# Optimization experiments

Measured on AMD Instinct MI355X. Metric: run time of the kernel, lower is better.

Reference implementation:

```python
import jax, jax.numpy as jnp
import numpy as np

N, C, H, W = 8, 256, 128, 128
HD = 256          # hidden_depth
FC, FS, CS = 8, 2, 8  # heads_count, fold_size, center_size
EPS_GN = 1e-5


def setup_inputs() -> dict:
    key = jax.random.key(0)
    ks = jax.random.split(key, 8)
    d = {
        'x': jax.random.normal(ks[0], (N, C, H, W), jnp.float32),
        'proj_w': jax.random.normal(ks[1], (2 * HD, C), jnp.float32) * 0.02,
        'proj_b': jnp.zeros((2 * HD,), jnp.float32),
        'merge_w': jax.random.normal(ks[2], (C, HD), jnp.float32) * 0.02,
        'merge_b': jnp.zeros((C,), jnp.float32),
        'alpha': jnp.ones((1,), jnp.float32),
        'beta': jnp.zeros((1,), jnp.float32),
        'g0_w': jnp.ones((C,), jnp.float32),
        'g0_b': jnp.zeros((C,), jnp.float32),
        'mlp_w0': jax.random.normal(ks[3], (2 * C, 2 * C), jnp.float32) * 0.02,
        'mlp_b0': jnp.zeros((2 * C,), jnp.float32),
        'mlp_w1': jax.random.normal(ks[4], (2 * C, C), jnp.float32) * 0.02,
        'mlp_b1': jnp.zeros((C,), jnp.float32),
        'g1_w': jnp.ones((C,), jnp.float32),
        'g1_b': jnp.zeros((C,), jnp.float32),
        'layer_scale': jnp.full((C,), 1e-5, jnp.float32),
    }
    return d


def _group_norm1(x, w, b):
    # GroupNorm(1, C): normalize over (C,H,W) per sample, per-channel affine
    mu = x.mean(axis=(1, 2, 3), keepdims=True)
    var = ((x - mu) ** 2).mean(axis=(1, 2, 3), keepdims=True)
    xn = (x - mu) * jax.lax.rsqrt(var + EPS_GN)
    return xn * w[None, :, None, None] + b[None, :, None, None]


def _l2norm(v):
    return v / jnp.maximum(jnp.linalg.norm(v, axis=-1, keepdims=True), 1e-12)


def _local_cluster(x, proj_w, proj_b, merge_w, merge_b, alpha, beta):
    n = x.shape[0]
    # 1x1 conv proj: C -> 2*HD
    y = jnp.einsum('nchw,oc->nohw', x, proj_w) + proj_b[None, :, None, None]
    c = y.shape[1] // FC              # per-head channels (2*HD/FC)
    h, w = H // FS, W // FS
    # 'n (fc c) (fh h) (fw w) -> (n fc fh fw) c h w'
    y = y.reshape(n, FC, c, FS, h, FS, w).transpose(0, 1, 3, 5, 2, 4, 6)
    y = y.reshape(n * FC * FS * FS, c, h, w)
    m = y.shape[0]
    # adaptive avg pool to CSxCS (h,w divisible by CS -> uniform pooling)
    center = y.reshape(m, c, CS, h // CS, CS, w // CS).mean(axis=(3, 5))
    L, s = h * w, CS * CS
    yf = y.reshape(m, c, L).transpose(0, 2, 1)       # [m, L, c]
    cf = center.reshape(m, c, s).transpose(0, 2, 1)  # [m, s, c]
    cv = c // 2
    x_point, x_value = yf[..., :cv], yf[..., cv:]
    c_point, c_value = cf[..., :cv], cf[..., cv:]
    sim = jnp.einsum('mlc,msc->mls', _l2norm(x_point), _l2norm(c_point))
    sim = jax.nn.sigmoid(alpha * sim + beta)         # [m, L, s]
    vals = sim.max(axis=2)                           # [m, L]
    idx = sim.argmax(axis=2) + s * jnp.arange(m)[:, None]
    vals = vals.reshape(-1)
    idx = idx.reshape(-1)
    xv = x_value.reshape(-1, cv)
    cvv = c_value.reshape(-1, cv)
    xv_aug = jnp.concatenate([xv, jnp.ones((xv.shape[0], 1), xv.dtype)], axis=1)
    cv_aug = jnp.concatenate([cvv, jnp.ones((cvv.shape[0], 1), cvv.dtype)], axis=1)
    # scatter-add weighted points into centers
    nc = cv_aug.at[idx].add(vals[:, None] * xv_aug)
    nc = nc[:, :-1] / nc[:, -1:]
    # gather back
    nx = vals[:, None] * nc[idx]                     # [m*L, cv]
    # '(n fc fh fw h w) c -> n (fc c) (fh h) (fw w)'
    nx = nx.reshape(n, FC, FS, FS, h, w, cv).transpose(0, 1, 6, 2, 4, 3, 5)
    nx = nx.reshape(n, FC * cv, H, W)                # [n, HD, H, W]
    return jnp.einsum('nchw,oc->nohw', nx, merge_w) + merge_b[None, :, None, None]


def reference(x, proj_w, proj_b, merge_w, merge_b, alpha, beta, g0_w, g0_b,
              mlp_w0, mlp_b0, mlp_w1, mlp_b1, g1_w, g1_b, layer_scale):
    new_x = _local_cluster(x, proj_w, proj_b, merge_w, merge_b, alpha, beta)
    new_x = _group_norm1(new_x, g0_w, g0_b)
    t = jnp.concatenate([x, new_x], axis=1)          # [n, 2C, H, W]
    t = t.transpose(0, 2, 3, 1)                      # NHWC
    t = jax.nn.gelu(t @ mlp_w0 + mlp_b0, approximate=False)
    t = t @ mlp_w1 + mlp_b1
    t = t.transpose(0, 3, 1, 2)                      # NCHW
    t = _group_norm1(t, g1_w, g1_b)
    t = t * layer_scale[None, :, None, None]
    return t + x
```

## Files before the change

### kernel.cpp

```cpp
#include <hip/hip_runtime.h>
#include <math.h>

#define PIX   16384
#define NB    8
#define CIN   256

typedef __attribute__((ext_vector_type(8))) short    short8;
typedef __attribute__((ext_vector_type(4))) float    f32x4;
typedef __attribute__((ext_vector_type(4))) unsigned short us4;
typedef __attribute__((ext_vector_type(8))) unsigned short us8;
typedef __attribute__((ext_vector_type(4))) unsigned char uc4;

__device__ __forceinline__ float bf2f(unsigned short h) {
  return __uint_as_float(((unsigned int)h) << 16);
}
__device__ __forceinline__ unsigned short f2bf(float f) {
  unsigned int u = __float_as_uint(f);
  return (unsigned short)((u + 0x7FFFu + ((u >> 16) & 1u)) >> 16);
}
__device__ __forceinline__ float gelu_f(float v) {
  return 0.5f * v * (1.f + erff(v * 0.70710678118654752f));
}

__device__ __forceinline__ unsigned fmono(float f) {
  const unsigned u = __float_as_uint(f);
  return (u & 0x80000000u) ? ~u : (u | 0x80000000u);
}

__device__ __forceinline__ unsigned umax16(unsigned v) {
  unsigned t;
  t = (unsigned)__builtin_amdgcn_update_dpp((int)v, (int)v, 0x121, 0xF, 0xF, false); v = v > t ? v : t;
  t = (unsigned)__builtin_amdgcn_update_dpp((int)v, (int)v, 0x122, 0xF, 0xF, false); v = v > t ? v : t;
  t = (unsigned)__builtin_amdgcn_update_dpp((int)v, (int)v, 0x124, 0xF, 0xF, false); v = v > t ? v : t;
  t = (unsigned)__builtin_amdgcn_update_dpp((int)v, (int)v, 0x128, 0xF, 0xF, false); v = v > t ? v : t;
  return v;
}
__device__ __forceinline__ int imin16(int v) {
  int t;
  t = __builtin_amdgcn_update_dpp(v, v, 0x121, 0xF, 0xF, false); v = v < t ? v : t;
  t = __builtin_amdgcn_update_dpp(v, v, 0x122, 0xF, 0xF, false); v = v < t ? v : t;
  t = __builtin_amdgcn_update_dpp(v, v, 0x124, 0xF, 0xF, false); v = v < t ? v : t;
  t = __builtin_amdgcn_update_dpp(v, v, 0x128, 0xF, 0xF, false); v = v < t ? v : t;
  return v;
}

__global__ void zero_kernel(float* p, int n) {
  int i = blockIdx.x * blockDim.x + threadIdx.x;
  if (i < n) p[i] = 0.f;
}

__global__ void prep_weights(const float* __restrict__ pw_f, const float* __restrict__ mw_f,
                             const float* __restrict__ w0, const float* __restrict__ w1,
                             unsigned short* __restrict__ pw, unsigned short* __restrict__ mw,
                             unsigned short* __restrict__ w0t, unsigned short* __restrict__ w1t) {
  const int S1 = 512 * 256, S2 = 256 * 256, S3 = 512 * 512, S4 = 256 * 512;
  int i = blockIdx.x * 256 + threadIdx.x;
  if (i < S1) { pw[i] = f2bf(pw_f[i]); return; }
  i -= S1;
  if (i < S2) { mw[i] = f2bf(mw_f[i]); return; }
  i -= S2;
  if (i < S3) { int o = i >> 9, k = i & 511; w0t[i] = f2bf(w0[k * 512 + o]); return; }
  i -= S3;
  if (i < S4) { int o = i >> 9, k = i & 511; w1t[i] = f2bf(w1[k * 256 + o]); }
}

__global__ __launch_bounds__(256) void x_to_nhwc(const float* __restrict__ x,
                                                 unsigned short* __restrict__ xT) {
  __shared__ float tile[64][65];
  const int t = threadIdx.x;
  const int p0 = blockIdx.x * 64, c0 = blockIdx.y * 64, n = blockIdx.z;
#pragma unroll
  for (int i = 0; i < 4; i++) {
    const int c = i * 16 + (t >> 4);
    const float4 v = *(const float4*)(x + ((size_t)(n * 256 + c0 + c) << 14) + p0 + (t & 15) * 4);
    tile[c][(t & 15) * 4]     = v.x;
    tile[c][(t & 15) * 4 + 1] = v.y;
    tile[c][(t & 15) * 4 + 2] = v.z;
    tile[c][(t & 15) * 4 + 3] = v.w;
  }
  __syncthreads();
#pragma unroll
  for (int i = 0; i < 4; i++) {
    const int pp = i * 16 + (t >> 4);
    const int cl = (t & 15) * 4;
    us4 o;
    o.x = f2bf(tile[cl][pp]); o.y = f2bf(tile[cl + 1][pp]);
    o.z = f2bf(tile[cl + 2][pp]); o.w = f2bf(tile[cl + 3][pp]);
    *(us4*)&xT[(((size_t)n << 14) + p0 + pp) * 256 + c0 + cl] = o;
  }
}

template<bool CONCAT, bool GELU, bool STATS>
__global__ __launch_bounds__(256, 4) void mfma_gemm(
    const unsigned short* __restrict__ A, const float* __restrict__ bias,
    const unsigned short* __restrict__ B1, const unsigned short* __restrict__ B2,
    unsigned short* __restrict__ Y, int M, int K, int K1,
    int astride, int bstride, float* __restrict__ sums) {
  __shared__ unsigned short As[8192];
  __shared__ unsigned short Bs[8192];
  __shared__ float r1[4], r2[4];
  const int t = threadIdx.x;
  const int lane = t & 63, w = t >> 6;
  const int quad = lane >> 4, l16 = lane & 15;
  const int p0 = blockIdx.x * 128, m0 = blockIdx.y * 128;
  const int n = blockIdx.z;
  const int wm = w & 1, wn = w >> 1;
  const int K2 = K - K1;

  A += (size_t)n * astride;

  f32x4 acc[4][4];
#pragma unroll
  for (int im = 0; im < 4; im++)
#pragma unroll
    for (int in = 0; in < 4; in++) acc[im][in] = (f32x4)0.f;

  for (int k0 = 0; k0 < K; k0 += 64) {
    __syncthreads();
#pragma unroll
    for (int i = 0; i < 4; i++) {
      const int c = (w << 2) | i;
      const int tm = c >> 1, kk = c & 1;
      const int krow = k0 + kk * 32 + quad * 8;
      const unsigned short* ga = A + (size_t)(m0 + tm * 16 + l16) * K + krow;
      __builtin_amdgcn_global_load_lds((const __attribute__((address_space(1))) void*)ga,
          (__attribute__((address_space(3))) void*)&As[c * 512], 16, 0, 0);
      const int prow = p0 + tm * 16 + l16;
      const unsigned short* gb;
      if (!CONCAT || krow < K1)
        gb = B1 + ((((size_t)n << 14) + prow) * (size_t)K1) + krow;
      else
        gb = B2 + ((((size_t)n << 14) + prow) * (size_t)K2) + (krow - K1);
      __builtin_amdgcn_global_load_lds((const __attribute__((address_space(1))) void*)gb,
          (__attribute__((address_space(3))) void*)&Bs[c * 512], 16, 0, 0);
    }
    __syncthreads();
#pragma unroll
    for (int kk = 0; kk < 2; kk++) {
      short8 af[4], bfr[4];
#pragma unroll
      for (int im = 0; im < 4; im++)
        af[im] = *(const short8*)&As[(((wm * 4 + im) * 2 + kk) * 64 + lane) * 8];
#pragma unroll
      for (int in = 0; in < 4; in++)
        bfr[in] = *(const short8*)&Bs[(((wn * 4 + in) * 2 + kk) * 64 + lane) * 8];
#pragma unroll
      for (int im = 0; im < 4; im++)
#pragma unroll
        for (int in = 0; in < 4; in++)
          acc[im][in] = __builtin_amdgcn_mfma_f32_16x16x32_bf16(af[im], bfr[in], acc[im][in], 0, 0, 0);
    }
  }

  const size_t nb = ((size_t)n << 14);
  float s = 0.f, s2 = 0.f;
#pragma unroll
  for (int im = 0; im < 4; im++) {
    const int om = m0 + (wm * 4 + im) * 16 + quad * 4;
    const f32x4 bv = *(const f32x4*)(bias + (size_t)n * bstride + om);
#pragma unroll
    for (int in = 0; in < 4; in++) {
      const int p = p0 + (wn * 4 + in) * 16 + l16;
      float v0 = acc[im][in].x + bv.x;
      float v1 = acc[im][in].y + bv.y;
      float v2 = acc[im][in].z + bv.z;
      float v3 = acc[im][in].w + bv.w;
      if (GELU) { v0 = gelu_f(v0); v1 = gelu_f(v1); v2 = gelu_f(v2); v3 = gelu_f(v3); }
      if (STATS) {
        s += (v0 + v1) + (v2 + v3);
        s2 = fmaf(v0, v0, s2); s2 = fmaf(v1, v1, s2);
        s2 = fmaf(v2, v2, s2); s2 = fmaf(v3, v3, s2);
      }
      us4 o4;
      o4.x = f2bf(v0); o4.y = f2bf(v1); o4.z = f2bf(v2); o4.w = f2bf(v3);
      *(us4*)&Y[(nb + p) * M + om] = o4;
    }
  }
  if (STATS) {
#pragma unroll
    for (int off = 32; off > 0; off >>= 1) {
      s += __shfl_down(s, off);
      s2 += __shfl_down(s2, off);
    }
    if (lane == 0) { r1[w] = s; r2[w] = s2; }
    __syncthreads();
    if (t == 0) {
      atomicAdd(&sums[2 * n],     (r1[0] + r1[1]) + (r1[2] + r1[3]));
      atomicAdd(&sums[2 * n + 1], (r2[0] + r2[1]) + (r2[2] + r2[3]));
    }
  }
}


__global__ __launch_bounds__(256) void centers_kernel(
    const unsigned short* __restrict__ y, unsigned short* __restrict__ cpnh_g,
    float* __restrict__ cval_g) {
  const int m = blockIdx.y, slice = blockIdx.x;
  const int n = m >> 5, f = (m >> 2) & 7, s1 = (m >> 1) & 1, s2 = m & 1;
  const int t = threadIdx.x;
  __shared__ float cs[16][68];

  const size_t nbase = ((size_t)n << 14);
  const int prow0 = s1 * 64, pcol0 = s2 * 64, ch0 = f * 64;

  {
    const int bl = t >> 4;
    const int b = slice * 16 + bl;
    const int tid = t & 15, cg = tid & 7, ph = tid >> 3;
    const int pr0 = prow0 + (b >> 3) * 8 + ph * 4;
    const int pc0 = pcol0 + (b & 7) * 8;
    const unsigned short* yb = y + (nbase + (size_t)pr0 * 128 + pc0) * 512 + ch0 + cg * 8;
    float a8[8] = {0.f, 0.f, 0.f, 0.f, 0.f, 0.f, 0.f, 0.f};
#pragma unroll
    for (int r = 0; r < 4; r++) {
      us8 buf[8];
#pragma unroll
      for (int cc = 0; cc < 8; cc++)
        buf[cc] = *(const us8*)(yb + ((size_t)r * 128 + cc) * 512);
#pragma unroll
      for (int cc = 0; cc < 8; cc++)
#pragma unroll
        for (int j = 0; j < 8; j++) a8[j] += bf2f(buf[cc][j]);
    }
#pragma unroll
    for (int j = 0; j < 8; j++) a8[j] += __shfl_xor(a8[j], 8);
    if (ph == 0) {
      f32x4 o0, o1;
      o0.x = a8[0] * (1.f / 64.f); o0.y = a8[1] * (1.f / 64.f);
      o0.z = a8[2] * (1.f / 64.f); o0.w = a8[3] * (1.f / 64.f);
      o1.x = a8[4] * (1.f / 64.f); o1.y = a8[5] * (1.f / 64.f);
      o1.z = a8[6] * (1.f / 64.f); o1.w = a8[7] * (1.f / 64.f);
      *(f32x4*)&cs[bl][cg * 8]     = o0;
      *(f32x4*)&cs[bl][cg * 8 + 4] = o1;
    }
  }
  __syncthreads();

  if (t < 128) {
    const int bl = t >> 3, jg = t & 7;
    const int bg = slice * 16 + bl;
    if (jg < 8) {
      f32x4 ov;
      ov.x = cs[bl][32 + jg * 4]; ov.y = cs[bl][32 + jg * 4 + 1];
      ov.z = cs[bl][32 + jg * 4 + 2]; ov.w = cs[bl][32 + jg * 4 + 3];
      *(f32x4*)&cval_g[((size_t)(m * 64 + bg) << 5) + jg * 4] = ov;
    }
    float s = 0.f;
#pragma unroll
    for (int cc = 0; cc < 32; cc++) { const float v = cs[bl][cc]; s = fmaf(v, v, s); }
    const float inv = 1.f / fmaxf(sqrtf(s), 1e-12f);
    us4 o;
    o.x = f2bf(cs[bl][jg * 4] * inv);     o.y = f2bf(cs[bl][jg * 4 + 1] * inv);
    o.z = f2bf(cs[bl][jg * 4 + 2] * inv); o.w = f2bf(cs[bl][jg * 4 + 3] * inv);
    *(us4*)&cpnh_g[((size_t)(m * 64 + bg) << 5) + jg * 4] = o;
  }
}

__global__ __launch_bounds__(256, 4) void assign_kernel(
    const unsigned short* __restrict__ y, const unsigned short* __restrict__ cpnh_g,
    const float* __restrict__ alpha_p, const float* __restrict__ beta_p,
    float* __restrict__ svals_g, unsigned char* __restrict__ sbest_g,
    float* __restrict__ accp_v, float* __restrict__ accp_c) {
  const int m = blockIdx.y, slice = blockIdx.x;
  const int n = m >> 5, f = (m >> 2) & 7, s1 = (m >> 1) & 1, s2 = m & 1;
  const int t = threadIdx.x;
  const int wave = t >> 6, lane = t & 63;
  const int quad = lane >> 4, l16 = lane & 15;
  const float alpha = alpha_p[0], beta = beta_p[0];

  __shared__ unsigned short yvs[512][34];
  __shared__ float svalss[512];
  __shared__ unsigned char sidxs[512];

  const size_t nbase = ((size_t)n << 14);
  const int prow0 = s1 * 64, pcol0 = s2 * 64, ch0 = f * 64;

  const short8 cb0 = *(const short8*)&cpnh_g[((size_t)(m * 64 +  0 + l16) << 5) + quad * 8];
  const short8 cb1 = *(const short8*)&cpnh_g[((size_t)(m * 64 + 16 + l16) << 5) + quad * 8];
  const short8 cb2 = *(const short8*)&cpnh_g[((size_t)(m * 64 + 32 + l16) << 5) + quad * 8];
  const short8 cb3 = *(const short8*)&cpnh_g[((size_t)(m * 64 + 48 + l16) << 5) + quad * 8];
  const int sl4 = (((l16 >> 2) << 4) | (l16 & 3)) << 2;

  auto loadpt = [&](int tile, short8& a, short8& v) {
    const int pidx = slice * 512 + wave * 128 + tile * 16;
    const int pix = (prow0 + (pidx >> 6)) * 128 + pcol0 + (pidx & 63) + l16;
    const unsigned short* yp = y + (nbase + pix) * 512 + ch0 + quad * 8;
    a = *(const short8*)yp;
    v = *(const short8*)(yp + 32);
  };

  auto compute_tile = [&](int tile, short8 apt, short8 avl) {
    const int pl = wave * 128 + tile * 16 + l16;
    const int pidx = slice * 512 + pl;

    float nrm = 0.f;
#pragma unroll
    for (int j = 0; j < 8; j++) {
      const float fv = bf2f((unsigned short)apt[j]);
      nrm = fmaf(fv, fv, nrm);
    }
    nrm += __shfl_xor(nrm, 16);
    nrm += __shfl_xor(nrm, 32);
    const float inva = 1.f / fmaxf(sqrtf(nrm), 1e-12f);

    const f32x4 d0 = __builtin_amdgcn_mfma_f32_16x16x32_bf16(apt, cb0, (f32x4)0.f, 0, 0, 0);
    const f32x4 d1 = __builtin_amdgcn_mfma_f32_16x16x32_bf16(apt, cb1, (f32x4)0.f, 0, 0, 0);
    const f32x4 d2 = __builtin_amdgcn_mfma_f32_16x16x32_bf16(apt, cb2, (f32x4)0.f, 0, 0, 0);
    const f32x4 d3 = __builtin_amdgcn_mfma_f32_16x16x32_bf16(apt, cb3, (f32x4)0.f, 0, 0, 0);

    float bv[4]; int bi[4];
#pragma unroll
    for (int r = 0; r < 4; r++) {
      const unsigned u0 = fmono(d0[r]);
      const unsigned u1 = fmono(d1[r]);
      const unsigned u2 = fmono(d2[r]);
      const unsigned u3 = fmono(d3[r]);
      unsigned mx = u0 > u1 ? u0 : u1;
      const unsigned mxb = u2 > u3 ? u2 : u3;
      mx = mx > mxb ? mx : mxb;
      mx = umax16(mx);
      int c0 = (u0 == mx) ? l16        : 64;
      int c1 = (u1 == mx) ? (16 + l16) : 64;
      int c2 = (u2 == mx) ? (32 + l16) : 64;
      int c3 = (u3 == mx) ? (48 + l16) : 64;
      int ci = c0 < c1 ? c0 : c1;
      const int cb = c2 < c3 ? c2 : c3;
      ci = ci < cb ? ci : cb;
      ci = imin16(ci);
      bi[r] = ci;
      bv[r] = __uint_as_float((mx & 0x80000000u) ? (mx ^ 0x80000000u) : ~mx);
    }

    const float rv01 = (l16 & 1) ? bv[1] : bv[0];
    const float rv23 = (l16 & 1) ? bv[3] : bv[2];
    const float rowv = (l16 & 2) ? rv23 : rv01;
    const int   ri01 = (l16 & 1) ? bi[1] : bi[0];
    const int   ri23 = (l16 & 1) ? bi[3] : bi[2];
    const int   rowi = (l16 & 2) ? ri23 : ri01;
    const unsigned pk = (__float_as_uint(rowv) & ~63u) | (unsigned)rowi;
    const unsigned got = (unsigned)__builtin_amdgcn_ds_bpermute(sl4, (int)pk);
    const int   idx = (int)(got & 63u);
    const float dot = __uint_as_float(got & ~63u);

    const float val = 1.f / (1.f + __expf(-fmaf(alpha, dot * inva, beta)));
    if (quad == 0) {
      svals_g[(size_t)m * 4096 + pidx + 0] = val;
      sbest_g[(size_t)m * 4096 + pidx + 0] = (unsigned char)idx;
      svalss[pl] = val;
      sidxs[pl] = (unsigned char)idx;
    }
    *(short8*)&yvs[pl][quad * 8] = avl;
  };

  {
    short8 a0, v0, a1, v1, a2, v2, a3, v3, a4, v4, a5, v5, a6, v6, a7, v7;
    loadpt(0, a0, v0); loadpt(1, a1, v1); loadpt(2, a2, v2); loadpt(3, a3, v3);
    loadpt(4, a4, v4); loadpt(5, a5, v5); loadpt(6, a6, v6); loadpt(7, a7, v7);
    compute_tile(0, a0, v0); compute_tile(1, a1, v1);
    compute_tile(2, a2, v2); compute_tile(3, a3, v3);
    compute_tile(4, a4, v4); compute_tile(5, a5, v5);
    compute_tile(6, a6, v6); compute_tile(7, a7, v7);
  }
  __syncthreads();

  {
    const int b = t >> 2, g = t & 3;
    float a8[8] = {0.f, 0.f, 0.f, 0.f, 0.f, 0.f, 0.f, 0.f};
    float ac = 0.f;
#pragma unroll 4
    for (int p4 = 0; p4 < 128; p4++) {
      const uc4 i4 = *(const uc4*)&sidxs[p4 * 4];
#pragma unroll
      for (int u = 0; u < 4; u++) {
        const int idx = (u == 0) ? i4.x : (u == 1) ? i4.y : (u == 2) ? i4.z : i4.w;
        if (idx == b) {
          const int p = p4 * 4 + u;
          const float val = svalss[p];
          const us8 yv = *(const us8*)&yvs[p][g * 8];
#pragma unroll
          for (int j = 0; j < 8; j++) a8[j] = fmaf(val, bf2f(yv[j]), a8[j]);
          ac += val;
        }
      }
    }
    const size_t pb = ((size_t)(m * 8 + slice)) * 64;
    f32x4 o0, o1;
    o0.x = a8[0]; o0.y = a8[1]; o0.z = a8[2]; o0.w = a8[3];
    o1.x = a8[4]; o1.y = a8[5]; o1.z = a8[6]; o1.w = a8[7];
    *(f32x4*)&accp_v[(pb + b) * 32 + g * 8]     = o0;
    *(f32x4*)&accp_v[(pb + b) * 32 + g * 8 + 4] = o1;
    if (g == 0) accp_c[pb + b] = ac;
  }
}

__global__ __launch_bounds__(256) void gather_kernel(
    const float* __restrict__ accp_v, const float* __restrict__ accp_c,
    const float* __restrict__ cval_g, const float* __restrict__ svals_g,
    const unsigned char* __restrict__ sbest_g, unsigned short* __restrict__ nx) {
  const int m = blockIdx.y, slice = blockIdx.x;
  const int n = m >> 5, f = (m >> 2) & 7, s1 = (m >> 1) & 1, s2 = m & 1;
  const int t = threadIdx.x;
  __shared__ float cm[64][34];

  const size_t nbase = ((size_t)n << 14);
  const int prow0 = s1 * 64, pcol0 = s2 * 64;

  for (int i = t; i < 2048; i += 256) {
    const int b = i >> 5, q = i & 31;
    float s = cval_g[((size_t)(m * 64 + b) << 5) + q];
    float c = 1.f;
#pragma unroll
    for (int s8 = 0; s8 < 8; s8++) {
      const size_t pb = ((size_t)(m * 8 + s8)) * 64 + b;
      s += accp_v[pb * 32 + q];
      c += accp_c[pb];
    }
    cm[b][q] = s / c;
  }
  __syncthreads();

#pragma unroll
  for (int pass = 0; pass < 2; pass++) {
    const int l = slice * 512 + pass * 256 + t;
    const int p = (prow0 + (l >> 6)) * 128 + pcol0 + (l & 63);
    const float v = svals_g[(size_t)m * 4096 + l];
    const int b = sbest_g[(size_t)m * 4096 + l];
    unsigned short* nr = nx + (nbase + p) * 256 + f * 32;
#pragma unroll
    for (int q8 = 0; q8 < 4; q8++) {
      const float2 a0 = *(const float2*)&cm[b][q8 * 8];
      const float2 a1 = *(const float2*)&cm[b][q8 * 8 + 2];
      const float2 a2 = *(const float2*)&cm[b][q8 * 8 + 4];
      const float2 a3 = *(const float2*)&cm[b][q8 * 8 + 6];
      us8 o;
      o[0] = f2bf(v * a0.x); o[1] = f2bf(v * a0.y);
      o[2] = f2bf(v * a1.x); o[3] = f2bf(v * a1.y);
      o[4] = f2bf(v * a2.x); o[5] = f2bf(v * a2.y);
      o[6] = f2bf(v * a3.x); o[7] = f2bf(v * a3.y);
      *(us8*)&nr[q8 * 8] = o;
    }
  }
}

__global__ void gn_finalize0(const float* __restrict__ sums, const float* __restrict__ g0w,
                             const float* __restrict__ g0b, float* __restrict__ scl,
                             float* __restrict__ bia) {
  const int n = blockIdx.x, c = threadIdx.x;
  const float cntinv = 1.f / (float)(CIN * PIX);
  const float mu = sums[2 * n] * cntinv;
  const float var = sums[2 * n + 1] * cntinv - mu * mu;
  const float rs = rsqrtf(var + 1e-5f);
  const float a = rs * g0w[c];
  scl[n * 256 + c] = a;
  bia[n * 256 + c] = g0b[c] - mu * a;
}

__global__ void w0_scale(const unsigned short* __restrict__ w0t,
                         const float* __restrict__ scl, unsigned short* __restrict__ w0s) {
  const int n = blockIdx.y;
  const int i = blockIdx.x * 256 + threadIdx.x;
  const int k = i & 511;
  unsigned short v = w0t[i];
  if (k >= 256) v = f2bf(bf2f(v) * scl[n * 256 + k - 256]);
  w0s[(size_t)n * 262144 + i] = v;
}

__global__ void b0_eff(const unsigned short* __restrict__ w0t, const float* __restrict__ b0,
                       const float* __restrict__ bia, float* __restrict__ b0e) {
  const int n = blockIdx.y;
  const int o = blockIdx.x * 256 + threadIdx.x;
  float s = b0[o];
  const unsigned short* wr = w0t + (size_t)o * 512 + 256;
  const float* br = bia + n * 256;
#pragma unroll 4
  for (int k = 0; k < 256; k++) s = fmaf(bf2f(wr[k]), br[k], s);
  b0e[n * 512 + o] = s;
}

__global__ __launch_bounds__(256) void final_transpose(
    const unsigned short* __restrict__ u, const float* __restrict__ x,
    const float* __restrict__ sums, const float* __restrict__ g1w,
    const float* __restrict__ g1b, const float* __restrict__ lsc,
    float* __restrict__ out) {
  __shared__ float tile[64][68];
  const int t = threadIdx.x;
  const int p0 = blockIdx.x * 64, c0 = blockIdx.y * 64, n = blockIdx.z;
  {
    const int pl = t >> 2, g = t & 3;
    const unsigned short* up = u + ((((size_t)n << 14) + p0 + pl) << 8) + c0 + g * 16;
    const us8 v0 = *(const us8*)up;
    const us8 v1 = *(const us8*)(up + 8);
#pragma unroll
    for (int j = 0; j < 8; j++) {
      tile[pl][g * 16 + j] = bf2f(v0[j]);
      tile[pl][g * 16 + 8 + j] = bf2f(v1[j]);
    }
  }
  __syncthreads();
  {
    const int cl = t >> 2, g = t & 3;
    const int c = c0 + cl;
    const float cntinv = 1.f / (float)(CIN * PIX);
    const float mu = sums[2 * n] * cntinv;
    const float var = sums[2 * n + 1] * cntinv - mu * mu;
    const float rs = rsqrtf(var + 1e-5f);
    const float gw = rs * g1w[c] * lsc[c];
    const float gb = (g1b[c] - mu * rs * g1w[c]) * lsc[c];
    const size_t rowb = ((size_t)(n * 256 + c) << 14) + p0 + g * 16;
#pragma unroll
    for (int q = 0; q < 4; q++) {
      const float4 xv = *(const float4*)(x + rowb + q * 4);
      float4 o;
      o.x = fmaf(tile[g * 16 + q * 4][cl], gw, gb) + xv.x;
      o.y = fmaf(tile[g * 16 + q * 4 + 1][cl], gw, gb) + xv.y;
      o.z = fmaf(tile[g * 16 + q * 4 + 2][cl], gw, gb) + xv.z;
      o.w = fmaf(tile[g * 16 + q * 4 + 3][cl], gw, gb) + xv.w;
      *(float4*)(out + rowb + q * 4) = o;
    }
  }
}

extern "C" void kernel_launch(void* const* d_in, const int* in_sizes, int n_in,
                              void* d_out, int out_size, void* d_ws, size_t ws_size,
                              hipStream_t stream) {
  const float* x       = (const float*)d_in[0];
  const float* proj_w  = (const float*)d_in[1];
  const float* proj_b  = (const float*)d_in[2];
  const float* merge_w = (const float*)d_in[3];
  const float* merge_b = (const float*)d_in[4];
  const float* alpha   = (const float*)d_in[5];
  const float* beta    = (const float*)d_in[6];
  const float* g0w     = (const float*)d_in[7];
  const float* g0b     = (const float*)d_in[8];
  const float* w0      = (const float*)d_in[9];
  const float* b0      = (const float*)d_in[10];
  const float* w1      = (const float*)d_in[11];
  const float* b1      = (const float*)d_in[12];
  const float* g1w     = (const float*)d_in[13];
  const float* g1b     = (const float*)d_in[14];
  const float* lsc     = (const float*)d_in[15];
  float* out = (float*)d_out;

  unsigned short* wsu = (unsigned short*)d_ws;
  unsigned short* xT  = wsu;
  unsigned short* y   = xT + (size_t)33554432;
  unsigned short* nx  = y + (size_t)67108864;
  unsigned short* pw  = nx + (size_t)33554432;
  unsigned short* mw  = pw + 131072;
  unsigned short* w0t = mw + 65536;
  unsigned short* w1t = w0t + 262144;
  unsigned short* w0s = w1t + 131072;
  float* sums = (float*)(w0s + (size_t)2097152);
  float* scl0 = sums + 32;
  float* bia0 = scl0 + 2048;
  float* b0e  = bia0 + 2048;
  unsigned short* newx = (unsigned short*)d_out;

  float* svals_g = (float*)((char*)d_out + 67108864);
  float* cval_g  = svals_g + 1048576;
  float* accp_v  = cval_g + 524288;
  float* accp_c  = accp_v + 4194304;
  unsigned short* cpnh_g = (unsigned short*)(accp_c + 131072);
  unsigned char*  sbest_g = (unsigned char*)(cpnh_g + 524288);

  zero_kernel<<<1, 64, 0, stream>>>(sums, 32);
  prep_weights<<<2304, 256, 0, stream>>>(proj_w, merge_w, w0, w1, pw, mw, w0t, w1t);
  x_to_nhwc<<<dim3(256, 4, NB), 256, 0, stream>>>(x, xT);

  mfma_gemm<false, false, false><<<dim3(128, 4, NB), 256, 0, stream>>>(
      pw, proj_b, xT, nullptr, y, 512, 256, 256, 0, 0, nullptr);

  centers_kernel<<<dim3(4, 256), 256, 0, stream>>>(y, cpnh_g, cval_g);
  assign_kernel<<<dim3(8, 256), 256, 0, stream>>>(
      y, cpnh_g, alpha, beta, svals_g, sbest_g, accp_v, accp_c);
  gather_kernel<<<dim3(8, 256), 256, 0, stream>>>(
      accp_v, accp_c, cval_g, svals_g, sbest_g, nx);

  mfma_gemm<false, false, true><<<dim3(128, 2, NB), 256, 0, stream>>>(
      mw, merge_b, nx, nullptr, newx, 256, 256, 256, 0, 0, sums);

  gn_finalize0<<<NB, 256, 0, stream>>>(sums, g0w, g0b, scl0, bia0);
  w0_scale<<<dim3(1024, NB), 256, 0, stream>>>(w0t, scl0, w0s);
  b0_eff<<<dim3(2, NB), 256, 0, stream>>>(w0t, b0, bia0, b0e);

  mfma_gemm<true, true, false><<<dim3(128, 4, NB), 256, 0, stream>>>(
      w0s, b0e, xT, newx, y, 512, 512, 256, 262144, 512, nullptr);

  mfma_gemm<false, false, true><<<dim3(128, 2, NB), 256, 0, stream>>>(
      w1t, b1, y, nullptr, nx, 256, 512, 512, 0, 0, sums + 16);

  final_transpose<<<dim3(256, 4, NB), 256, 0, stream>>>(
      nx, x, sums + 16, g1w, g1b, lsc, out);
}
```

Measured before the change: 915.4 us.

## Fuse projection GEMM into cluster assign kernel and compute centers from pooled input

```diff
diff --git a/kernel.cpp b/kernel.cpp
--- a/kernel.cpp
+++ b/kernel.cpp
@@ -52,8 +52,9 @@
 __global__ void prep_weights(const float* __restrict__ pw_f, const float* __restrict__ mw_f,
                              const float* __restrict__ w0, const float* __restrict__ w1,
                              unsigned short* __restrict__ pw, unsigned short* __restrict__ mw,
-                             unsigned short* __restrict__ w0t, unsigned short* __restrict__ w1t) {
-  const int S1 = 512 * 256, S2 = 256 * 256, S3 = 512 * 512, S4 = 256 * 512;
+                             unsigned short* __restrict__ w0t, unsigned short* __restrict__ w1t,
+                             unsigned short* __restrict__ pwF) {
+  const int S1 = 512 * 256, S2 = 256 * 256, S3 = 512 * 512, S4 = 256 * 512, S5 = 512 * 256;
   int i = blockIdx.x * 256 + threadIdx.x;
   if (i < S1) { pw[i] = f2bf(pw_f[i]); return; }
   i -= S1;
@@ -61,7 +62,14 @@
   i -= S2;
   if (i < S3) { int o = i >> 9, k = i & 511; w0t[i] = f2bf(w0[k * 512 + o]); return; }
   i -= S3;
-  if (i < S4) { int o = i >> 9, k = i & 511; w1t[i] = f2bf(w1[k * 256 + o]); }
+  if (i < S4) { int o = i >> 9, k = i & 511; w1t[i] = f2bf(w1[k * 256 + o]); return; }
+  i -= S4;
+  if (i < S5) {
+    const int j = i & 7, lane = (i >> 3) & 63, ks = (i >> 9) & 7, ct = (i >> 12) & 3, f = i >> 14;
+    const int ch = f * 64 + ct * 16 + (lane & 15);
+    const int k  = ks * 32 + (lane >> 4) * 8 + j;
+    pwF[i] = f2bf(pw_f[ch * 256 + k]);
+  }
 }
 
 __global__ __launch_bounds__(256) void x_to_nhwc(const float* __restrict__ x,
@@ -192,72 +200,94 @@
 }
 
 
+__global__ __launch_bounds__(256) void xmeans_kernel(
+    const unsigned short* __restrict__ xT, float* __restrict__ xmean) {
+  const int reg = blockIdx.y, ksl = blockIdx.x;
+  const int nn = reg >> 2, s1 = (reg >> 1) & 1, s2 = reg & 1;
+  const int t = threadIdx.x;
+  const int b = t >> 2, kq = t & 3;
+  const int k0 = ksl * 64 + kq * 16;
+  const size_t nbase = ((size_t)nn << 14);
+  const int pr0 = s1 * 64 + (b >> 3) * 8, pc0 = s2 * 64 + (b & 7) * 8;
+  float a16[16];
+#pragma unroll
+  for (int j = 0; j < 16; j++) a16[j] = 0.f;
+#pragma unroll 1
+  for (int r = 0; r < 8; r++) {
+#pragma unroll
+    for (int c = 0; c < 8; c++) {
+      const unsigned short* xp = xT + (nbase + (size_t)(pr0 + r) * 128 + pc0 + c) * 256 + k0;
+      const us8 v0 = *(const us8*)xp;
+      const us8 v1 = *(const us8*)(xp + 8);
+#pragma unroll
+      for (int j = 0; j < 8; j++) {
+        a16[j]     += bf2f(v0[j]);
+        a16[8 + j] += bf2f(v1[j]);
+      }
+    }
+  }
+  float* o = xmean + (((size_t)(reg * 64 + b)) << 8) + k0;
+#pragma unroll
+  for (int j = 0; j < 16; j++) o[j] = a16[j] * (1.f / 64.f);
+}
+
 __global__ __launch_bounds__(256) void centers_kernel(
-    const unsigned short* __restrict__ y, unsigned short* __restrict__ cpnh_g,
+    const float* __restrict__ xmean, const unsigned short* __restrict__ pw,
+    const float* __restrict__ proj_bp, unsigned short* __restrict__ cpnh_g,
     float* __restrict__ cval_g) {
-  const int m = blockIdx.y, slice = blockIdx.x;
-  const int n = m >> 5, f = (m >> 2) & 7, s1 = (m >> 1) & 1, s2 = m & 1;
+  const int m = blockIdx.x;
+  const int nn = m >> 5, f = (m >> 2) & 7, s1 = (m >> 1) & 1, s2 = m & 1;
+  const int reg = (nn << 2) | (s1 << 1) | s2;
   const int t = threadIdx.x;
-  __shared__ float cs[16][68];
-
-  const size_t nbase = ((size_t)n << 14);
-  const int prow0 = s1 * 64, pcol0 = s2 * 64, ch0 = f * 64;
+  const int b = t >> 2, cg = t & 3;
+  __shared__ float cs[64][68];
 
   {
-    const int bl = t >> 4;
-    const int b = slice * 16 + bl;
-    const int tid = t & 15, cg = tid & 7, ph = tid >> 3;
-    const int pr0 = prow0 + (b >> 3) * 8 + ph * 4;
-    const int pc0 = pcol0 + (b & 7) * 8;
-    const unsigned short* yb = y + (nbase + (size_t)pr0 * 128 + pc0) * 512 + ch0 + cg * 8;
-    float a8[8] = {0.f, 0.f, 0.f, 0.f, 0.f, 0.f, 0.f, 0.f};
-#pragma unroll
-    for (int r = 0; r < 4; r++) {
-      us8 buf[8];
-#pragma unroll
-      for (int cc = 0; cc < 8; cc++)
-        buf[cc] = *(const us8*)(yb + ((size_t)r * 128 + cc) * 512);
-#pragma unroll
-      for (int cc = 0; cc < 8; cc++)
-#pragma unroll
-        for (int j = 0; j < 8; j++) a8[j] += bf2f(buf[cc][j]);
-    }
-#pragma unroll
-    for (int j = 0; j < 8; j++) a8[j] += __shfl_xor(a8[j], 8);
-    if (ph == 0) {
-      f32x4 o0, o1;
-      o0.x = a8[0] * (1.f / 64.f); o0.y = a8[1] * (1.f / 64.f);
-      o0.z = a8[2] * (1.f / 64.f); o0.w = a8[3] * (1.f / 64.f);
-      o1.x = a8[4] * (1.f / 64.f); o1.y = a8[5] * (1.f / 64.f);
-      o1.z = a8[6] * (1.f / 64.f); o1.w = a8[7] * (1.f / 64.f);
-      *(f32x4*)&cs[bl][cg * 8]     = o0;
-      *(f32x4*)&cs[bl][cg * 8 + 4] = o1;
-    }
+    const float* xm = xmean + (((size_t)(reg * 64 + b)) << 8);
+    float acc16[16];
+#pragma unroll
+    for (int c = 0; c < 16; c++) acc16[c] = 0.f;
+#pragma unroll 1
+    for (int k = 0; k < 256; k += 8) {
+      float xv[8];
+#pragma unroll
+      for (int j = 0; j < 8; j++) xv[j] = xm[k + j];
+#pragma unroll
+      for (int c = 0; c < 16; c++) {
+        const us8 wv = *(const us8*)(pw + (size_t)(f * 64 + cg * 16 + c) * 256 + k);
+#pragma unroll
+        for (int j = 0; j < 8; j++) acc16[c] = fmaf(bf2f(wv[j]), xv[j], acc16[c]);
+      }
+    }
+#pragma unroll
+    for (int c = 0; c < 16; c++)
+      cs[b][cg * 16 + c] = acc16[c] + proj_bp[f * 64 + cg * 16 + c];
   }
   __syncthreads();
 
-  if (t < 128) {
-    const int bl = t >> 3, jg = t & 7;
-    const int bg = slice * 16 + bl;
-    if (jg < 8) {
-      f32x4 ov;
-      ov.x = cs[bl][32 + jg * 4]; ov.y = cs[bl][32 + jg * 4 + 1];
-      ov.z = cs[bl][32 + jg * 4 + 2]; ov.w = cs[bl][32 + jg * 4 + 3];
-      *(f32x4*)&cval_g[((size_t)(m * 64 + bg) << 5) + jg * 4] = ov;
-    }
+  {
+    const int b2 = t >> 2, jg = t & 3;
+    const f32x4 ov0 = *(const f32x4*)&cs[b2][32 + jg * 8];
+    const f32x4 ov1 = *(const f32x4*)&cs[b2][32 + jg * 8 + 4];
+    *(f32x4*)&cval_g[(((size_t)(m * 64 + b2)) << 5) + jg * 8]     = ov0;
+    *(f32x4*)&cval_g[(((size_t)(m * 64 + b2)) << 5) + jg * 8 + 4] = ov1;
     float s = 0.f;
 #pragma unroll
-    for (int cc = 0; cc < 32; cc++) { const float v = cs[bl][cc]; s = fmaf(v, v, s); }
+    for (int cc = 0; cc < 32; cc++) { const float v = cs[b2][cc]; s = fmaf(v, v, s); }
     const float inv = 1.f / fmaxf(sqrtf(s), 1e-12f);
-    us4 o;
-    o.x = f2bf(cs[bl][jg * 4] * inv);     o.y = f2bf(cs[bl][jg * 4 + 1] * inv);
-    o.z = f2bf(cs[bl][jg * 4 + 2] * inv); o.w = f2bf(cs[bl][jg * 4 + 3] * inv);
-    *(us4*)&cpnh_g[((size_t)(m * 64 + bg) << 5) + jg * 4] = o;
-  }
-}
-
-__global__ __launch_bounds__(256, 4) void assign_kernel(
-    const unsigned short* __restrict__ y, const unsigned short* __restrict__ cpnh_g,
+    us4 o0, o1;
+    o0.x = f2bf(cs[b2][jg * 8] * inv);     o0.y = f2bf(cs[b2][jg * 8 + 1] * inv);
+    o0.z = f2bf(cs[b2][jg * 8 + 2] * inv); o0.w = f2bf(cs[b2][jg * 8 + 3] * inv);
+    o1.x = f2bf(cs[b2][jg * 8 + 4] * inv); o1.y = f2bf(cs[b2][jg * 8 + 5] * inv);
+    o1.z = f2bf(cs[b2][jg * 8 + 6] * inv); o1.w = f2bf(cs[b2][jg * 8 + 7] * inv);
+    *(us4*)&cpnh_g[(((size_t)(m * 64 + b2)) << 5) + jg * 8]     = o0;
+    *(us4*)&cpnh_g[(((size_t)(m * 64 + b2)) << 5) + jg * 8 + 4] = o1;
+  }
+}
+
+__global__ __launch_bounds__(256, 3) void assign_kernel(
+    const unsigned short* __restrict__ xT, const unsigned short* __restrict__ pwF,
+    const float* __restrict__ proj_bp, const unsigned short* __restrict__ cpnh_g,
     const float* __restrict__ alpha_p, const float* __restrict__ beta_p,
     float* __restrict__ svals_g, unsigned char* __restrict__ sbest_g,
     float* __restrict__ accp_v, float* __restrict__ accp_c) {
@@ -268,12 +298,12 @@
   const int quad = lane >> 4, l16 = lane & 15;
   const float alpha = alpha_p[0], beta = beta_p[0];
 
-  __shared__ unsigned short yvs[512][34];
-  __shared__ float svalss[512];
-  __shared__ unsigned char sidxs[512];
+  __shared__ unsigned short ytile[16][2][64][8];
+  __shared__ float svalss[256];
+  __shared__ unsigned char sidxs[256];
 
   const size_t nbase = ((size_t)n << 14);
-  const int prow0 = s1 * 64, pcol0 = s2 * 64, ch0 = f * 64;
+  const int prow0 = s1 * 64, pcol0 = s2 * 64;
 
   const short8 cb0 = *(const short8*)&cpnh_g[((size_t)(m * 64 +  0 + l16) << 5) + quad * 8];
   const short8 cb1 = *(const short8*)&cpnh_g[((size_t)(m * 64 + 16 + l16) << 5) + quad * 8];
@@ -281,17 +311,59 @@
   const short8 cb3 = *(const short8*)&cpnh_g[((size_t)(m * 64 + 48 + l16) << 5) + quad * 8];
   const int sl4 = (((l16 >> 2) << 4) | (l16 & 3)) << 2;
 
-  auto loadpt = [&](int tile, short8& a, short8& v) {
-    const int pidx = slice * 512 + wave * 128 + tile * 16;
-    const int pix = (prow0 + (pidx >> 6)) * 128 + pcol0 + (pidx & 63) + l16;
-    const unsigned short* yp = y + (nbase + pix) * 512 + ch0 + quad * 8;
-    a = *(const short8*)yp;
-    v = *(const short8*)(yp + 32);
-  };
-
-  auto compute_tile = [&](int tile, short8 apt, short8 avl) {
-    const int pl = wave * 128 + tile * 16 + l16;
-    const int pidx = slice * 512 + pl;
+  float pb[4];
+#pragma unroll
+  for (int ct = 0; ct < 4; ct++) pb[ct] = proj_bp[f * 64 + ct * 16 + l16];
+
+  {
+    f32x4 acc[4][4];
+#pragma unroll
+    for (int pt = 0; pt < 4; pt++)
+#pragma unroll
+      for (int ct = 0; ct < 4; ct++) acc[pt][ct] = (f32x4)0.f;
+    const unsigned short* pwb = pwF + ((size_t)f << 14);
+#pragma unroll 1
+    for (int ks = 0; ks < 8; ks++) {
+      short8 af[4], bf_[4];
+#pragma unroll
+      for (int pt = 0; pt < 4; pt++) {
+        const int pidx = slice * 256 + wave * 64 + pt * 16;
+        const int pix = (prow0 + (pidx >> 6)) * 128 + pcol0 + (pidx & 63) + l16;
+        af[pt] = *(const short8*)(xT + (nbase + pix) * (size_t)256 + ks * 32 + quad * 8);
+      }
+#pragma unroll
+      for (int ct = 0; ct < 4; ct++)
+        bf_[ct] = *(const short8*)(pwb + ((ct * 8 + ks) * 64 + lane) * 8);
+#pragma unroll
+      for (int pt = 0; pt < 4; pt++)
+#pragma unroll
+        for (int ct = 0; ct < 4; ct++)
+          acc[pt][ct] = __builtin_amdgcn_mfma_f32_16x16x32_bf16(af[pt], bf_[ct], acc[pt][ct], 0, 0, 0);
+    }
+#pragma unroll
+    for (int pt = 0; pt < 4; pt++) {
+      const int tileG = wave * 4 + pt;
+#pragma unroll
+      for (int ct = 0; ct < 4; ct++) {
+        const int ch = ct * 16 + l16;
+        const int half = ch >> 5, chm = ch & 31;
+        const int dq = chm >> 3, j = chm & 7;
+#pragma unroll
+        for (int r = 0; r < 4; r++) {
+          const float v = acc[pt][ct][r] + pb[ct];
+          ytile[tileG][half][dq * 16 + (quad * 4 + r)][j] = f2bf(v);
+        }
+      }
+    }
+  }
+  __syncthreads();
+
+#pragma unroll 1
+  for (int tt = 0; tt < 4; tt++) {
+    const int tile = wave * 4 + tt;
+    const short8 apt = *(const short8*)&ytile[tile][0][quad * 16 + l16][0];
+    const short8 avl = *(const short8*)&ytile[tile][1][quad * 16 + l16][0];
+    (void)avl;
 
     float nrm = 0.f;
 #pragma unroll
@@ -344,22 +416,12 @@
 
     const float val = 1.f / (1.f + __expf(-fmaf(alpha, dot * inva, beta)));
     if (quad == 0) {
-      svals_g[(size_t)m * 4096 + pidx + 0] = val;
-      sbest_g[(size_t)m * 4096 + pidx + 0] = (unsigned char)idx;
-      svalss[pl] = val;
-      sidxs[pl] = (unsigned char)idx;
-    }
-    *(short8*)&yvs[pl][quad * 8] = avl;
-  };
-
-  {
-    short8 a0, v0, a1, v1, a2, v2, a3, v3, a4, v4, a5, v5, a6, v6, a7, v7;
-    loadpt(0, a0, v0); loadpt(1, a1, v1); loadpt(2, a2, v2); loadpt(3, a3, v3);
-    loadpt(4, a4, v4); loadpt(5, a5, v5); loadpt(6, a6, v6); loadpt(7, a7, v7);
-    compute_tile(0, a0, v0); compute_tile(1, a1, v1);
-    compute_tile(2, a2, v2); compute_tile(3, a3, v3);
-    compute_tile(4, a4, v4); compute_tile(5, a5, v5);
-    compute_tile(6, a6, v6); compute_tile(7, a7, v7);
+      const int pidxg = slice * 256 + tile * 16 + l16;
+      svals_g[(size_t)m * 4096 + pidxg] = val;
+      sbest_g[(size_t)m * 4096 + pidxg] = (unsigned char)idx;
+      svalss[tile * 16 + l16] = val;
+      sidxs[tile * 16 + l16] = (unsigned char)idx;
+    }
   }
   __syncthreads();
 
@@ -368,7 +430,7 @@
     float a8[8] = {0.f, 0.f, 0.f, 0.f, 0.f, 0.f, 0.f, 0.f};
     float ac = 0.f;
 #pragma unroll 4
-    for (int p4 = 0; p4 < 128; p4++) {
+    for (int p4 = 0; p4 < 64; p4++) {
       const uc4 i4 = *(const uc4*)&sidxs[p4 * 4];
 #pragma unroll
       for (int u = 0; u < 4; u++) {
@@ -376,20 +438,20 @@
         if (idx == b) {
           const int p = p4 * 4 + u;
           const float val = svalss[p];
-          const us8 yv = *(const us8*)&yvs[p][g * 8];
+          const us8 yv = *(const us8*)&ytile[p >> 4][1][(g << 4) | (p & 15)][0];
 #pragma unroll
           for (int j = 0; j < 8; j++) a8[j] = fmaf(val, bf2f(yv[j]), a8[j]);
           ac += val;
         }
       }
     }
-    const size_t pb = ((size_t)(m * 8 + slice)) * 64;
+    const size_t pbx = ((size_t)(m * 16 + slice)) * 64;
     f32x4 o0, o1;
     o0.x = a8[0]; o0.y = a8[1]; o0.z = a8[2]; o0.w = a8[3];
     o1.x = a8[4]; o1.y = a8[5]; o1.z = a8[6]; o1.w = a8[7];
-    *(f32x4*)&accp_v[(pb + b) * 32 + g * 8]     = o0;
-    *(f32x4*)&accp_v[(pb + b) * 32 + g * 8 + 4] = o1;
-    if (g == 0) accp_c[pb + b] = ac;
+    *(f32x4*)&accp_v[(pbx + b) * 32 + g * 8]     = o0;
+    *(f32x4*)&accp_v[(pbx + b) * 32 + g * 8 + 4] = o1;
+    if (g == 0) accp_c[pbx + b] = ac;
   }
 }
 
@@ -410,10 +472,10 @@
     float s = cval_g[((size_t)(m * 64 + b) << 5) + q];
     float c = 1.f;
 #pragma unroll
-    for (int s8 = 0; s8 < 8; s8++) {
-      const size_t pb = ((size_t)(m * 8 + s8)) * 64 + b;
-      s += accp_v[pb * 32 + q];
-      c += accp_c[pb];
+    for (int s16 = 0; s16 < 16; s16++) {
+      const size_t pbx = ((size_t)(m * 16 + s16)) * 64 + b;
+      s += accp_v[pbx * 32 + q];
+      c += accp_c[pbx];
     }
     cm[b][q] = s / c;
   }
@@ -554,25 +616,25 @@
   float* scl0 = sums + 32;
   float* bia0 = scl0 + 2048;
   float* b0e  = bia0 + 2048;
+  unsigned short* pwF = (unsigned short*)(b0e + 4096);
+  float* xmean = (float*)y;
   unsigned short* newx = (unsigned short*)d_out;
 
   float* svals_g = (float*)((char*)d_out + 67108864);
   float* cval_g  = svals_g + 1048576;
   float* accp_v  = cval_g + 524288;
-  float* accp_c  = accp_v + 4194304;
-  unsigned short* cpnh_g = (unsigned short*)(accp_c + 131072);
+  float* accp_c  = accp_v + 8388608;
+  unsigned short* cpnh_g = (unsigned short*)(accp_c + 262144);
   unsigned char*  sbest_g = (unsigned char*)(cpnh_g + 524288);
 
   zero_kernel<<<1, 64, 0, stream>>>(sums, 32);
-  prep_weights<<<2304, 256, 0, stream>>>(proj_w, merge_w, w0, w1, pw, mw, w0t, w1t);
+  prep_weights<<<2816, 256, 0, stream>>>(proj_w, merge_w, w0, w1, pw, mw, w0t, w1t, pwF);
   x_to_nhwc<<<dim3(256, 4, NB), 256, 0, stream>>>(x, xT);
 
-  mfma_gemm<false, false, false><<<dim3(128, 4, NB), 256, 0, stream>>>(
-      pw, proj_b, xT, nullptr, y, 512, 256, 256, 0, 0, nullptr);
-
-  centers_kernel<<<dim3(4, 256), 256, 0, stream>>>(y, cpnh_g, cval_g);
-  assign_kernel<<<dim3(8, 256), 256, 0, stream>>>(
-      y, cpnh_g, alpha, beta, svals_g, sbest_g, accp_v, accp_c);
+  xmeans_kernel<<<dim3(4, 32), 256, 0, stream>>>(xT, xmean);
+  centers_kernel<<<256, 256, 0, stream>>>(xmean, pw, proj_b, cpnh_g, cval_g);
+  assign_kernel<<<dim3(16, 256), 256, 0, stream>>>(
+      xT, pwF, proj_b, cpnh_g, alpha, beta, svals_g, sbest_g, accp_v, accp_c);
   gather_kernel<<<dim3(8, 256), 256, 0, stream>>>(
       accp_v, accp_c, cval_g, svals_g, sbest_g, nx);
 
```

Result: slower. 936.7 us (+2.3%).
